# Kernel optimization log

Hardware: AMD Instinct MI355X
Metric: run time of the kernel (lower is better)

## Reference

```python
import jax, jax.numpy as jnp
import numpy as np
import math

EPS = 1e-5  # BatchNorm eps; eval mode with running_mean=0, running_var=1


def maxpool(x, k, p):
    return jax.lax.reduce_window(x, -jnp.inf, jax.lax.max,
                                 (1, 1, k, k), (1, 1, 1, 1),
                                 ((0, 0), (0, 0), (p, p), (p, p)))


def conv1x1(x, w, b=None):
    # x: [B,Cin,H,W], w: [Cout,Cin]
    y = jnp.einsum('oi,bihw->bohw', w, x)
    if b is not None:
        y = y + b[None, :, None, None]
    return y


def bn_eval(x, g, b):
    scale = g / jnp.sqrt(1.0 + EPS)
    return x * scale[None, :, None, None] + b[None, :, None, None]


def setup_inputs() -> dict:
    B, C, H, W = 2, 64, 80, 80
    c1, c2, c3 = 21, 21, 22
    ch = 32  # C//2
    ks = jax.random.split(jax.random.key(0), 16)
    s = 0.05
    inp = {
        'x': jax.random.normal(ks[0], (B, C, H, W), jnp.float32),
        'q1_w': jax.random.normal(ks[1], (c1, c1), jnp.float32) * s,
        'q1_g': jnp.ones((c1,), jnp.float32),
        'q1_b': jnp.zeros((c1,), jnp.float32),
        'q2_w': jax.random.normal(ks[2], (c2, c2), jnp.float32) * s,
        'q2_g': jnp.ones((c2,), jnp.float32),
        'q2_b': jnp.zeros((c2,), jnp.float32),
        'q3_w': jax.random.normal(ks[3], (c3, c3), jnp.float32) * s,
        'q3_g': jnp.ones((c3,), jnp.float32),
        'q3_b': jnp.zeros((c3,), jnp.float32),
        'k_hf_w': jax.random.normal(ks[4], (ch, C), jnp.float32) * s,
        'k_hf_b': jnp.zeros((ch,), jnp.float32),
        'k_lf_w': jax.random.normal(ks[5], (C - ch, C), jnp.float32) * s,
        'k_lf_b': jnp.zeros((C - ch,), jnp.float32),
        'k_fuse_w': jax.random.normal(ks[6], (C, C), jnp.float32) * s,
        'k_fuse_b': jnp.zeros((C,), jnp.float32),
        'v_bn_g': jnp.ones((C,), jnp.float32),
        'v_bn_b': jnp.zeros((C,), jnp.float32),
        'v_w': jax.random.normal(ks[7], (C, C), jnp.float32) * s,
        'v_b': jnp.zeros((C,), jnp.float32),
        'out_w': jax.random.normal(ks[8], (C, C), jnp.float32) * s,
        'out_b': jnp.zeros((C,), jnp.float32),
    }
    return inp


def reference(x, q1_w, q1_g, q1_b, q2_w, q2_g, q2_b, q3_w, q3_g, q3_b,
              k_hf_w, k_hf_b, k_lf_w, k_lf_b, k_fuse_w, k_fuse_b,
              v_bn_g, v_bn_b, v_w, v_b, out_w, out_b):
    B, C, H, W = x.shape
    N = H * W
    c1 = q1_w.shape[0]
    c2 = q2_w.shape[0]
    # Q: ThreeGroupConvQ (split -> 1x1 conv (no bias) -> BN -> ReLU -> concat)
    x1, x2, x3 = jnp.split(x, [c1, c1 + c2], axis=1)
    y1 = jax.nn.relu(bn_eval(conv1x1(x1, q1_w), q1_g, q1_b))
    y2 = jax.nn.relu(bn_eval(conv1x1(x2, q2_w), q2_g, q2_b))
    y3 = jax.nn.relu(bn_eval(conv1x1(x3, q3_w), q3_g, q3_b))
    Q = jnp.concatenate([y1, y2, y3], axis=1)
    # K: ThermalStructureExtractor
    p3 = maxpool(x, 3, 1)
    p5 = maxpool(x, 5, 2)
    low = (p3 + p5) * 0.5
    high = conv1x1(x - low, k_hf_w, k_hf_b)
    lowp = conv1x1(low, k_lf_w, k_lf_b)
    K = conv1x1(jnp.concatenate([high, lowp], axis=1), k_fuse_w, k_fuse_b)
    # V: BN -> 1x1 conv
    V = conv1x1(bn_eval(x, v_bn_g, v_bn_b), v_w, v_b)
    # attention over N = H*W spatial tokens, channel features
    Qc = Q.reshape(B, C, N)
    Kc = K.reshape(B, C, N)
    Vc = V.reshape(B, C, N)
    attn = jax.nn.softmax(
        jnp.einsum('bcn,bcm->bnm', Qc, Kc) / math.sqrt(C), axis=-1)  # [B,N,N]
    out = jnp.einsum('bnm,bcm->bcn', attn, Vc).reshape(B, C, H, W)
    return conv1x1(out, out_w, out_b) + x
```

## Files before the change

kernel.cpp:

```cpp
#include <hip/hip_runtime.h>
#include <hip/hip_bf16.h>


#define BATCH 2
#define CH 64
#define HH 80
#define WW 80
#define NN 6400
#define NT 100
#define KS 10
#define KTPS (NT/KS)
#define EPSV 1e-5f
#define NEGBIG (-1e30f)
#define QP 72
#define LOG2E8 0.18033688f
#define VSP 65

typedef __hip_bfloat16 bf16;
typedef __attribute__((ext_vector_type(8))) short short8;
typedef __attribute__((ext_vector_type(4))) float f4;
#define MFMA16 __builtin_amdgcn_mfma_f32_16x16x32_bf16

__device__ __forceinline__ float b2f(bf16 v){ return __bfloat162float(v); }
__device__ __forceinline__ bf16 f2b(float v){ return __float2bfloat16(v); }
__device__ __forceinline__ ushort f2bu(float v){ return ((__hip_bfloat16_raw)__float2bfloat16(v)).x; }
__device__ __forceinline__ float bu2f(ushort u){
  union { unsigned int i; float f; } w; w.i = ((unsigned int)u) << 16; return w.f;
}
__device__ __forceinline__ unsigned pkbf(float a, float b){
  union { __hip_bfloat162 h2; unsigned u; } cv;
  cv.h2 = __float22bfloat162_rn(make_float2(a, b));
  return cv.u;
}
__device__ __forceinline__ float fexp2(float x){
#if __has_builtin(__builtin_amdgcn_exp2f)
  return __builtin_amdgcn_exp2f(x);
#else
  return exp2f(x);
#endif
}

#define OFF_BIAS 0
#define OFF_WH_B 768
#define OFF_LOW_B (768 + 32768)
#define OFF_Q_B   (OFF_LOW_B + BATCH*CH*NN*2)
#define OFF_K_B   (OFF_Q_B   + BATCH*CH*NN*2)
#define OFF_V_B   (OFF_K_B   + BATCH*CH*NN*2)
#define OFF_P_B   (OFF_V_B   + BATCH*CH*NN*2)
#define OFF_ML_B  (OFF_P_B   + BATCH*NT*KS*4096*2)

__global__ __launch_bounds__(256) void setup_fold(
    const float* __restrict__ q1w, const float* __restrict__ q1g, const float* __restrict__ q1b,
    const float* __restrict__ q2w, const float* __restrict__ q2g, const float* __restrict__ q2b,
    const float* __restrict__ q3w, const float* __restrict__ q3g, const float* __restrict__ q3b,
    const float* __restrict__ khw, const float* __restrict__ khb,
    const float* __restrict__ klw, const float* __restrict__ klb,
    const float* __restrict__ kfw, const float* __restrict__ kfb,
    const float* __restrict__ vg,  const float* __restrict__ vbnb,
    const float* __restrict__ vw,  const float* __restrict__ vb,
    const float* __restrict__ outw,
    float* __restrict__ biasf, bf16* __restrict__ wh)
{
  __shared__ __align__(16) float skf[4096];
  __shared__ __align__(16) float skh[2048];
  __shared__ __align__(16) float skl[2048];
  __shared__ __align__(16) float sow[4096];
  __shared__ __align__(16) float svw[4096];
  __shared__ float sbv[64];

  int tid = threadIdx.x;
  int blk = blockIdx.x;
  #pragma unroll
  for (int i = 0; i < 4; ++i) {
    *(float4*)&skf[(i*256 + tid)*4] = *(const float4*)&kfw[(i*256 + tid)*4];
    *(float4*)&sow[(i*256 + tid)*4] = *(const float4*)&outw[(i*256 + tid)*4];
    *(float4*)&svw[(i*256 + tid)*4] = *(const float4*)&vw[(i*256 + tid)*4];
  }
  #pragma unroll
  for (int i = 0; i < 2; ++i) {
    *(float4*)&skh[(i*256 + tid)*4] = *(const float4*)&khw[(i*256 + tid)*4];
    *(float4*)&skl[(i*256 + tid)*4] = *(const float4*)&klw[(i*256 + tid)*4];
  }
  __syncthreads();

  float rs = rsqrtf(1.0f + EPSV);
  if (tid < 64) {
    int j = tid;
    float bvo = vb[j];
    for (int ci2 = 0; ci2 < 64; ++ci2) bvo += svw[j*64 + ci2] * vbnb[ci2];
    sbv[j] = bvo;
  }

  bf16* wq   = wh;
  bf16* wvp  = wh + 4096;
  bf16* wa1  = wh + 8192;
  bf16* wa2m = wh + 12288;

  int t = blk*256 + tid;
  int ci = t & 63, co = t >> 6;
  int o = ci*64 + co;

  float w = 0.f, g;
  if (co < 21)      { g = q1g[co];    w = (ci < 21)              ? q1w[co*21 + ci]            : 0.f; }
  else if (co < 42) { g = q2g[co-21]; w = (ci >= 21 && ci < 42)  ? q2w[(co-21)*21 + (ci-21)]  : 0.f; }
  else              { g = q3g[co-42]; w = (ci >= 42)             ? q3w[(co-42)*22 + (ci-42)]  : 0.f; }
  wq[o] = f2b(w * g * rs * LOG2E8);

  float a1 = 0.f, a2 = 0.f;
  #pragma unroll
  for (int j = 0; j < 32; ++j) {
    a1 += skf[co*64 + j]      * skh[j*64 + ci];
    a2 += skf[co*64 + 32 + j] * skl[j*64 + ci];
  }
  wa1[o]  = f2b(a1);
  wa2m[o] = f2b(a2 - a1);

  float av = 0.f;
  #pragma unroll
  for (int j = 0; j < 64; ++j)
    av += sow[co*64 + j] * svw[j*64 + ci];
  wvp[o] = f2b(av * vg[ci] * rs);

  if (blk == 0 && tid < 64) {
    int c2 = tid;
    float bq;
    if (c2 < 21)      bq = q1b[c2];
    else if (c2 < 42) bq = q2b[c2-21];
    else              bq = q3b[c2-42];
    biasf[c2] = bq * LOG2E8;
    float bk = kfb[c2];
    #pragma unroll
    for (int j = 0; j < 32; ++j) {
      bk += skf[c2*64 + j]      * khb[j];
      bk += skf[c2*64 + 32 + j] * klb[j];
    }
    biasf[64 + c2] = bk;
    __syncthreads();
  }
  __syncthreads();
  if (blk == 0 && tid < 64) {
    int c2 = tid;
    float bvp = 0.f;
    #pragma unroll
    for (int j = 0; j < 64; ++j) bvp += sow[c2*64 + j] * sbv[j];
    biasf[128 + c2] = bvp;
  }
}

__global__ __launch_bounds__(256) void pool_low(const float* __restrict__ x,
                                                bf16* __restrict__ lowg)
{
  int t4 = (blockIdx.x*256 + threadIdx.x)*4;
  int bc = t4 / NN; int n = t4 % NN;
  int h = n / WW, w0 = n % WW;
  const float* p = x + bc*NN;
  float m5[4], m3[4];
  #pragma unroll
  for (int j=0;j<4;++j){ m5[j]=NEGBIG; m3[j]=NEGBIG; }
  #pragma unroll
  for (int dh = -2; dh <= 2; ++dh) {
    int hh = h + dh; if (hh < 0 || hh >= HH) continue;
    float r[12];
    const float* row = p + hh*WW;
    if (w0 >= 4)      { float4 a = *(const float4*)&row[w0-4]; r[0]=a.x;r[1]=a.y;r[2]=a.z;r[3]=a.w; }
    else              { r[0]=NEGBIG;r[1]=NEGBIG;r[2]=NEGBIG;r[3]=NEGBIG; }
    { float4 a = *(const float4*)&row[w0]; r[4]=a.x;r[5]=a.y;r[6]=a.z;r[7]=a.w; }
    if (w0 + 7 < WW)  { float4 a = *(const float4*)&row[w0+4]; r[8]=a.x;r[9]=a.y;r[10]=a.z;r[11]=a.w; }
    else              { r[8]=NEGBIG;r[9]=NEGBIG;r[10]=NEGBIG;r[11]=NEGBIG; }
    bool in3 = (dh >= -1 && dh <= 1);
    #pragma unroll
    for (int j=0;j<4;++j) {
      float v3 = fmaxf(fmaxf(r[3+j], r[4+j]), r[5+j]);
      float v5 = fmaxf(fmaxf(r[2+j], v3), r[6+j]);
      m5[j] = fmaxf(m5[j], v5);
      if (in3) m3[j] = fmaxf(m3[j], v3);
    }
  }
  ushort4 o;
  o.x = f2bu(0.5f*(m3[0]+m5[0]));
  o.y = f2bu(0.5f*(m3[1]+m5[1]));
  o.z = f2bu(0.5f*(m3[2]+m5[2]));
  o.w = f2bu(0.5f*(m3[3]+m5[3]));
  *(ushort4*)&lowg[t4] = o;
}

__global__ __launch_bounds__(256) void qkv_kernel(
    const float* __restrict__ x, const float* __restrict__ biasf,
    const bf16* __restrict__ wh, const bf16* __restrict__ lowg,
    bf16* __restrict__ qgT, bf16* __restrict__ kgT, bf16* __restrict__ vgc)
{
  __shared__ __align__(16) float xs[64*32];
  __shared__ __align__(16) float lows[64*32];
  __shared__ __align__(16) bf16  wbuf[16384];
  __shared__ ushort vs[64*VSP];
  __shared__ float bias[192];

  int tid = threadIdx.x;
  int blk = blockIdx.x;
  int b = blk / (NT*2);
  int rem = blk % (NT*2);
  int tile = rem >> 1, half = rem & 1;
  int n0 = tile*64 + half*32;

  #pragma unroll
  for (int i = 0; i < 8; ++i) {
    int e = i*256 + tid; int c = e >> 5, p = e & 31;
    xs[c*32 + p]   = x[(b*CH + c)*NN + n0 + p];
    lows[c*32 + p] = b2f(lowg[(b*CH + c)*NN + n0 + p]);
  }
  #pragma unroll
  for (int i = 0; i < 16; ++i)
    ((uint2*)wbuf)[i*256 + tid] = ((const uint2*)wh)[i*256 + tid];
  if (tid < 192) bias[tid] = biasf[tid];
  __syncthreads();

  int co = tid & 63, pg = tid >> 6;
  const bf16* wq   = wbuf;
  const bf16* wvp  = wbuf + 4096;
  const bf16* wa1  = wbuf + 8192;
  const bf16* wa2m = wbuf + 12288;

  {
    float bq = bias[co];
    float4 a0 = make_float4(bq,bq,bq,bq), a1v = a0;
    for (int ci = 0; ci < 64; ++ci) {
      float wv = b2f(wq[ci*64 + co]);
      float4 x0 = *(const float4*)&xs[ci*32 + pg*8];
      float4 x1 = *(const float4*)&xs[ci*32 + pg*8 + 4];
      a0.x += wv*x0.x; a0.y += wv*x0.y; a0.z += wv*x0.z; a0.w += wv*x0.w;
      a1v.x += wv*x1.x; a1v.y += wv*x1.y; a1v.z += wv*x1.z; a1v.w += wv*x1.w;
    }
    float q8[8] = {a0.x,a0.y,a0.z,a0.w,a1v.x,a1v.y,a1v.z,a1v.w};
    #pragma unroll
    for (int j=0;j<8;++j)
      qgT[(size_t)(b*NN + n0 + pg*8 + j)*64 + co] = f2b(fmaxf(q8[j], 0.f));
  }
  {
    float bv = bias[128 + co];
    float4 a0 = make_float4(bv,bv,bv,bv), a1v = a0;
    for (int ci = 0; ci < 64; ++ci) {
      float wv = b2f(wvp[ci*64 + co]);
      float4 x0 = *(const float4*)&xs[ci*32 + pg*8];
      float4 x1 = *(const float4*)&xs[ci*32 + pg*8 + 4];
      a0.x += wv*x0.x; a0.y += wv*x0.y; a0.z += wv*x0.z; a0.w += wv*x0.w;
      a1v.x += wv*x1.x; a1v.y += wv*x1.y; a1v.z += wv*x1.z; a1v.w += wv*x1.w;
    }
    float v8[8] = {a0.x,a0.y,a0.z,a0.w,a1v.x,a1v.y,a1v.z,a1v.w};
    #pragma unroll
    for (int j=0;j<8;++j)
      vs[co*VSP + pg*8 + j] = f2bu(v8[j]);
  }
  __syncthreads();
  {
    int c = tid >> 2, cb = (tid & 3)*8;
    ushort u[8];
    #pragma unroll
    for (int j=0;j<8;++j) u[j] = vs[c*VSP + cb + j];
    uint4 pk;
    pk.x = (uint)u[0] | ((uint)u[1] << 16);
    pk.y = (uint)u[2] | ((uint)u[3] << 16);
    pk.z = (uint)u[4] | ((uint)u[5] << 16);
    pk.w = (uint)u[6] | ((uint)u[7] << 16);
    *(uint4*)&vgc[(size_t)(b*CH + c)*NN + n0 + cb] = pk;
  }
  {
    float bk = bias[64 + co];
    float4 a0 = make_float4(bk,bk,bk,bk), a1v = a0;
    for (int ci = 0; ci < 64; ++ci) {
      float w1 = b2f(wa1[ci*64 + co]);
      float w2 = b2f(wa2m[ci*64 + co]);
      float4 x0 = *(const float4*)&xs[ci*32 + pg*8];
      float4 x1 = *(const float4*)&xs[ci*32 + pg*8 + 4];
      float4 l0 = *(const float4*)&lows[ci*32 + pg*8];
      float4 l1 = *(const float4*)&lows[ci*32 + pg*8 + 4];
      a0.x += w1*x0.x + w2*l0.x; a0.y += w1*x0.y + w2*l0.y;
      a0.z += w1*x0.z + w2*l0.z; a0.w += w1*x0.w + w2*l0.w;
      a1v.x += w1*x1.x + w2*l1.x; a1v.y += w1*x1.y + w2*l1.y;
      a1v.z += w1*x1.z + w2*l1.z; a1v.w += w1*x1.w + w2*l1.w;
    }
    float k8[8] = {a0.x,a0.y,a0.z,a0.w,a1v.x,a1v.y,a1v.z,a1v.w};
    #pragma unroll
    for (int j=0;j<8;++j)
      kgT[(size_t)(b*NN + n0 + pg*8 + j)*64 + co] = f2b(k8[j]);
  }
}

__global__ __launch_bounds__(256) void attn_partial(
    const bf16* __restrict__ qgT, const bf16* __restrict__ kgT, const bf16* __restrict__ vgc,
    ushort* __restrict__ part, float* __restrict__ pml)
{
  __shared__ __align__(16) char smem[27648];
  __shared__ float lred[256];
  bf16* Qld = (bf16*)smem;
  bf16* Pld = (bf16*)smem;
  bf16* Kld = (bf16*)(smem + 9216);
  bf16* Vld = (bf16*)(smem + 18432);

  int tid = threadIdx.x;
  int blk = blockIdx.x;
  int b = blk / (NT*KS);
  int rem = blk % (NT*KS);
  int tile = rem / KS, split = rem % KS;
  int n0 = tile*64;
  int wv = tid >> 6, lane = tid & 63, ln = lane & 15, quad = lane >> 4;
  int arow = (wv*16 + ln)*QP;

  #pragma unroll
  for (int i = 0; i < 4; ++i) {
    int f = (i*256 + tid)*4; int n = f >> 6, c = f & 63;
    *(uint2*)&Qld[n*QP + c] = *(const uint2*)&qgT[(size_t)(b*NN + n0 + n)*64 + c];
  }
  __syncthreads();
  short8 bq[4][2];
  #pragma unroll
  for (int nt = 0; nt < 4; ++nt) {
    bq[nt][0] = *(const short8*)&Qld[(nt*16 + ln)*QP + quad*8];
    bq[nt][1] = *(const short8*)&Qld[(nt*16 + ln)*QP + 32 + quad*8];
  }

  f4 accO[4];
  float lacc[4];
  #pragma unroll
  for (int t=0;t<4;++t) accO[t] = (f4){0.f,0.f,0.f,0.f};
  #pragma unroll
  for (int nt=0;nt<4;++nt) lacc[nt] = 0.f;

  uint2 kreg[4], vreg[4];
  int mbase = split*KTPS*64;
  #pragma unroll
  for (int i = 0; i < 4; ++i) {
    int f = (i*256 + tid)*4; int rr = f >> 6, cc = f & 63;
    kreg[i] = *(const uint2*)&kgT[(size_t)(b*NN + mbase + rr)*64 + cc];
    vreg[i] = *(const uint2*)&vgc[(size_t)(b*CH + rr)*NN + mbase + cc];
  }

  for (int kt = 0; kt < KTPS; ++kt) {
    __syncthreads();
    #pragma unroll
    for (int i = 0; i < 4; ++i) {
      int f = (i*256 + tid)*4; int rr = f >> 6, cc = f & 63;
      *(uint2*)&Kld[rr*QP + cc] = kreg[i];
      *(uint2*)&Vld[rr*QP + cc] = vreg[i];
    }
    __syncthreads();
    if (kt + 1 < KTPS) {
      int m0 = mbase + (kt+1)*64;
      #pragma unroll
      for (int i = 0; i < 4; ++i) {
        int f = (i*256 + tid)*4; int rr = f >> 6, cc = f & 63;
        kreg[i] = *(const uint2*)&kgT[(size_t)(b*NN + m0 + rr)*64 + cc];
        vreg[i] = *(const uint2*)&vgc[(size_t)(b*CH + rr)*NN + m0 + cc];
      }
    }

    short8 ak0 = *(const short8*)&Kld[arow + quad*8];
    short8 ak1 = *(const short8*)&Kld[arow + 32 + quad*8];
    f4 accS[4];
    #pragma unroll
    for (int nt = 0; nt < 4; ++nt) {
      f4 z = (f4){0.f,0.f,0.f,0.f};
      z = MFMA16(ak0, bq[nt][0], z, 0, 0, 0);
      accS[nt] = MFMA16(ak1, bq[nt][1], z, 0, 0, 0);
    }
    #pragma unroll
    for (int nt = 0; nt < 4; ++nt) {
      float p0 = fexp2(accS[nt][0]), p1 = fexp2(accS[nt][1]);
      float p2 = fexp2(accS[nt][2]), p3 = fexp2(accS[nt][3]);
      lacc[nt] += (p0 + p1) + (p2 + p3);
      uint2 pk;
      pk.x = pkbf(p0, p1);
      pk.y = pkbf(p2, p3);
      *(uint2*)&Pld[(nt*16 + ln)*QP + wv*16 + quad*4] = pk;
    }
    __syncthreads();

    short8 ap0 = *(const short8*)&Pld[arow + quad*8];
    short8 ap1 = *(const short8*)&Pld[arow + 32 + quad*8];
    #pragma unroll
    for (int t = 0; t < 4; ++t) {
      short8 bv0 = *(const short8*)&Vld[(t*16+ln)*QP + quad*8];
      short8 bv1 = *(const short8*)&Vld[(t*16+ln)*QP + 32 + quad*8];
      accO[t] = MFMA16(ap0, bv0, accO[t], 0, 0, 0);
      accO[t] = MFMA16(ap1, bv1, accO[t], 0, 0, 0);
    }
  }

  size_t pbase = ((size_t)(b*NT + tile)*KS + split)*4096;
  ushort* pp = part + pbase;
  #pragma unroll
  for (int t = 0; t < 4; ++t) {
    uint2 pk;
    pk.x = pkbf(accO[t][0], accO[t][1]);
    pk.y = pkbf(accO[t][2], accO[t][3]);
    *(uint2*)&pp[(t*16 + ln)*64 + wv*16 + quad*4] = pk;
  }
  #pragma unroll
  for (int nt = 0; nt < 4; ++nt) {
    float s = lacc[nt];
    s += __shfl_xor(s, 16);
    s += __shfl_xor(s, 32);
    if (quad == 0) lred[wv*64 + nt*16 + ln] = s;
  }
  __syncthreads();
  if (tid < 64) {
    size_t mlb = ((size_t)(b*NT + tile)*KS + split)*64;
    pml[mlb + tid] = (lred[tid] + lred[64 + tid]) + (lred[128 + tid] + lred[192 + tid]);
  }
}

__global__ __launch_bounds__(256) void attn_reduce(
    const ushort* __restrict__ part, const float* __restrict__ pml,
    const float* __restrict__ x, const float* __restrict__ outb,
    float* __restrict__ out)
{
  __shared__ float linv[64];
  __shared__ float ob[64];

  int tid = threadIdx.x;
  int blk = blockIdx.x;
  int b = blk / NT, tile = blk % NT;
  size_t base = (size_t)(b*NT + tile)*KS;

  if (tid < 64) {
    float l = 0.f;
    #pragma unroll
    for (int s=0;s<KS;++s) l += pml[(base+s)*64 + tid];
    linv[tid] = 1.0f / l;
    ob[tid] = outb[tid];
  }
  __syncthreads();

  #pragma unroll
  for (int j = 0; j < 4; ++j) {
    int idx = j*256 + tid;
    int c = idx >> 4, q = idx & 15;
    float a0=0.f, a1=0.f, a2=0.f, a3=0.f;
    #pragma unroll
    for (int s = 0; s < KS; ++s) {
      uint2 v = *(const uint2*)&part[(base+s)*4096 + (size_t)c*64 + q*4];
      a0 += bu2f((ushort)(v.x & 0xffff)); a1 += bu2f((ushort)(v.x >> 16));
      a2 += bu2f((ushort)(v.y & 0xffff)); a3 += bu2f((ushort)(v.y >> 16));
    }
    int nl = q*4;
    size_t gidx = (size_t)(b*CH + c)*NN + tile*64 + nl;
    float4 xv = *(const float4*)&x[gidx];
    float bc = ob[c];
    float4 o;
    o.x = a0*linv[nl+0] + bc + xv.x;
    o.y = a1*linv[nl+1] + bc + xv.y;
    o.z = a2*linv[nl+2] + bc + xv.z;
    o.w = a3*linv[nl+3] + bc + xv.w;
    *(float4*)&out[gidx] = o;
  }
}

extern "C" void kernel_launch(void* const* d_in, const int* in_sizes, int n_in,
                              void* d_out, int out_size, void* d_ws, size_t ws_size,
                              hipStream_t stream) {
  const float* x    = (const float*)d_in[0];
  const float* q1w  = (const float*)d_in[1];
  const float* q1g  = (const float*)d_in[2];
  const float* q1b  = (const float*)d_in[3];
  const float* q2w  = (const float*)d_in[4];
  const float* q2g  = (const float*)d_in[5];
  const float* q2b  = (const float*)d_in[6];
  const float* q3w  = (const float*)d_in[7];
  const float* q3g  = (const float*)d_in[8];
  const float* q3b  = (const float*)d_in[9];
  const float* khw  = (const float*)d_in[10];
  const float* khb  = (const float*)d_in[11];
  const float* klw  = (const float*)d_in[12];
  const float* klb  = (const float*)d_in[13];
  const float* kfw  = (const float*)d_in[14];
  const float* kfb  = (const float*)d_in[15];
  const float* vbg  = (const float*)d_in[16];
  const float* vbb  = (const float*)d_in[17];
  const float* vw   = (const float*)d_in[18];
  const float* vb   = (const float*)d_in[19];
  const float* outw = (const float*)d_in[20];
  const float* outb = (const float*)d_in[21];

  char*   wsb  = (char*)d_ws;
  float*  biasf= (float*)(wsb + OFF_BIAS);
  bf16*   wh   = (bf16*)(wsb + OFF_WH_B);
  bf16*   lowg = (bf16*)(wsb + OFF_LOW_B);
  bf16*   qgT  = (bf16*)(wsb + OFF_Q_B);
  bf16*   kgT  = (bf16*)(wsb + OFF_K_B);
  bf16*   vgc  = (bf16*)(wsb + OFF_V_B);
  ushort* part = (ushort*)(wsb + OFF_P_B);
  float*  pml  = (float*)(wsb + OFF_ML_B);

  hipLaunchKernelGGL(setup_fold, dim3(16), dim3(256), 0, stream,
                     q1w,q1g,q1b,q2w,q2g,q2b,q3w,q3g,q3b,
                     khw,khb,klw,klb,kfw,kfb,vbg,vbb,vw,vb,outw, biasf, wh);
  hipLaunchKernelGGL(pool_low, dim3(BATCH*CH*NN/1024), dim3(256), 0, stream, x, lowg);
  hipLaunchKernelGGL(qkv_kernel, dim3(BATCH*NT*2), dim3(256), 0, stream,
                     x, biasf, wh, lowg, qgT, kgT, vgc);
  hipLaunchKernelGGL(attn_partial, dim3(BATCH*NT*KS), dim3(256), 0, stream,
                     qgT, kgT, vgc, part, pml);
  hipLaunchKernelGGL(attn_reduce, dim3(BATCH*NT), dim3(256), 0, stream,
                     part, pml, x, outb, (float*)d_out);
}
```

Before: 171.2 us.

## Fuse attention split-K partials and reduction into one 1024-thread block kernel

```diff
diff --git a/kernel.cpp b/kernel.cpp
--- a/kernel.cpp
+++ b/kernel.cpp
@@ -8,13 +8,15 @@
 #define WW 80
 #define NN 6400
 #define NT 100
-#define KS 10
-#define KTPS (NT/KS)
+#define NG 4
+#define KTPS 25
 #define EPSV 1e-5f
 #define NEGBIG (-1e30f)
 #define QP 72
 #define LOG2E8 0.18033688f
 #define VSP 65
+#define GREG 27648
+#define OPF 65
 
 typedef __hip_bfloat16 bf16;
 typedef __attribute__((ext_vector_type(8))) short short8;
@@ -24,9 +26,6 @@
 __device__ __forceinline__ float b2f(bf16 v){ return __bfloat162float(v); }
 __device__ __forceinline__ bf16 f2b(float v){ return __float2bfloat16(v); }
 __device__ __forceinline__ ushort f2bu(float v){ return ((__hip_bfloat16_raw)__float2bfloat16(v)).x; }
-__device__ __forceinline__ float bu2f(ushort u){
-  union { unsigned int i; float f; } w; w.i = ((unsigned int)u) << 16; return w.f;
-}
 __device__ __forceinline__ unsigned pkbf(float a, float b){
   union { __hip_bfloat162 h2; unsigned u; } cv;
   cv.h2 = __float22bfloat162_rn(make_float2(a, b));
@@ -46,10 +45,9 @@
 #define OFF_Q_B   (OFF_LOW_B + BATCH*CH*NN*2)
 #define OFF_K_B   (OFF_Q_B   + BATCH*CH*NN*2)
 #define OFF_V_B   (OFF_K_B   + BATCH*CH*NN*2)
-#define OFF_P_B   (OFF_V_B   + BATCH*CH*NN*2)
-#define OFF_ML_B  (OFF_P_B   + BATCH*NT*KS*4096*2)
-
-__global__ __launch_bounds__(256) void setup_fold(
+
+__global__ __launch_bounds__(256) void setup_pool(
+    const float* __restrict__ x,
     const float* __restrict__ q1w, const float* __restrict__ q1g, const float* __restrict__ q1b,
     const float* __restrict__ q2w, const float* __restrict__ q2g, const float* __restrict__ q2b,
     const float* __restrict__ q3w, const float* __restrict__ q3g, const float* __restrict__ q3b,
@@ -59,129 +57,104 @@
     const float* __restrict__ vg,  const float* __restrict__ vbnb,
     const float* __restrict__ vw,  const float* __restrict__ vb,
     const float* __restrict__ outw,
-    float* __restrict__ biasf, bf16* __restrict__ wh)
+    float* __restrict__ biasf, bf16* __restrict__ wh, bf16* __restrict__ lowg)
 {
-  __shared__ __align__(16) float skf[4096];
-  __shared__ __align__(16) float skh[2048];
-  __shared__ __align__(16) float skl[2048];
-  __shared__ __align__(16) float sow[4096];
-  __shared__ __align__(16) float svw[4096];
   __shared__ float sbv[64];
-
   int tid = threadIdx.x;
   int blk = blockIdx.x;
-  #pragma unroll
-  for (int i = 0; i < 4; ++i) {
-    *(float4*)&skf[(i*256 + tid)*4] = *(const float4*)&kfw[(i*256 + tid)*4];
-    *(float4*)&sow[(i*256 + tid)*4] = *(const float4*)&outw[(i*256 + tid)*4];
-    *(float4*)&svw[(i*256 + tid)*4] = *(const float4*)&vw[(i*256 + tid)*4];
-  }
-  #pragma unroll
-  for (int i = 0; i < 2; ++i) {
-    *(float4*)&skh[(i*256 + tid)*4] = *(const float4*)&khw[(i*256 + tid)*4];
-    *(float4*)&skl[(i*256 + tid)*4] = *(const float4*)&klw[(i*256 + tid)*4];
-  }
-  __syncthreads();
-
-  float rs = rsqrtf(1.0f + EPSV);
-  if (tid < 64) {
-    int j = tid;
-    float bvo = vb[j];
-    for (int ci2 = 0; ci2 < 64; ++ci2) bvo += svw[j*64 + ci2] * vbnb[ci2];
-    sbv[j] = bvo;
-  }
-
-  bf16* wq   = wh;
-  bf16* wvp  = wh + 4096;
-  bf16* wa1  = wh + 8192;
-  bf16* wa2m = wh + 12288;
-
-  int t = blk*256 + tid;
-  int ci = t & 63, co = t >> 6;
-  int o = ci*64 + co;
-
-  float w = 0.f, g;
-  if (co < 21)      { g = q1g[co];    w = (ci < 21)              ? q1w[co*21 + ci]            : 0.f; }
-  else if (co < 42) { g = q2g[co-21]; w = (ci >= 21 && ci < 42)  ? q2w[(co-21)*21 + (ci-21)]  : 0.f; }
-  else              { g = q3g[co-42]; w = (ci >= 42)             ? q3w[(co-42)*22 + (ci-42)]  : 0.f; }
-  wq[o] = f2b(w * g * rs * LOG2E8);
-
-  float a1 = 0.f, a2 = 0.f;
-  #pragma unroll
-  for (int j = 0; j < 32; ++j) {
-    a1 += skf[co*64 + j]      * skh[j*64 + ci];
-    a2 += skf[co*64 + 32 + j] * skl[j*64 + ci];
-  }
-  wa1[o]  = f2b(a1);
-  wa2m[o] = f2b(a2 - a1);
-
-  float av = 0.f;
-  #pragma unroll
-  for (int j = 0; j < 64; ++j)
-    av += sow[co*64 + j] * svw[j*64 + ci];
-  wvp[o] = f2b(av * vg[ci] * rs);
-
-  if (blk == 0 && tid < 64) {
-    int c2 = tid;
-    float bq;
-    if (c2 < 21)      bq = q1b[c2];
-    else if (c2 < 42) bq = q2b[c2-21];
-    else              bq = q3b[c2-42];
-    biasf[c2] = bq * LOG2E8;
-    float bk = kfb[c2];
-    #pragma unroll
+
+  if (blk < 16) {
+    float rs = rsqrtf(1.0f + EPSV);
+    bf16* wq   = wh;
+    bf16* wvp  = wh + 4096;
+    bf16* wa1  = wh + 8192;
+    bf16* wa2m = wh + 12288;
+
+    int t = blk*256 + tid;
+    int ci = t & 63, co = t >> 6;
+    int o = ci*64 + co;
+
+    float w = 0.f, g;
+    if (co < 21)      { g = q1g[co];    w = (ci < 21)              ? q1w[co*21 + ci]            : 0.f; }
+    else if (co < 42) { g = q2g[co-21]; w = (ci >= 21 && ci < 42)  ? q2w[(co-21)*21 + (ci-21)]  : 0.f; }
+    else              { g = q3g[co-42]; w = (ci >= 42)             ? q3w[(co-42)*22 + (ci-42)]  : 0.f; }
+    wq[o] = f2b(w * g * rs * LOG2E8);
+
+    float a1 = 0.f, a2 = 0.f, av = 0.f;
+    #pragma unroll 8
     for (int j = 0; j < 32; ++j) {
-      bk += skf[c2*64 + j]      * khb[j];
-      bk += skf[c2*64 + 32 + j] * klb[j];
-    }
-    biasf[64 + c2] = bk;
-    __syncthreads();
-  }
-  __syncthreads();
-  if (blk == 0 && tid < 64) {
-    int c2 = tid;
-    float bvp = 0.f;
-    #pragma unroll
-    for (int j = 0; j < 64; ++j) bvp += sow[c2*64 + j] * sbv[j];
-    biasf[128 + c2] = bvp;
-  }
-}
-
-__global__ __launch_bounds__(256) void pool_low(const float* __restrict__ x,
-                                                bf16* __restrict__ lowg)
-{
-  int t4 = (blockIdx.x*256 + threadIdx.x)*4;
-  int bc = t4 / NN; int n = t4 % NN;
-  int h = n / WW, w0 = n % WW;
-  const float* p = x + bc*NN;
-  float m5[4], m3[4];
-  #pragma unroll
-  for (int j=0;j<4;++j){ m5[j]=NEGBIG; m3[j]=NEGBIG; }
-  #pragma unroll
-  for (int dh = -2; dh <= 2; ++dh) {
-    int hh = h + dh; if (hh < 0 || hh >= HH) continue;
-    float r[12];
-    const float* row = p + hh*WW;
-    if (w0 >= 4)      { float4 a = *(const float4*)&row[w0-4]; r[0]=a.x;r[1]=a.y;r[2]=a.z;r[3]=a.w; }
-    else              { r[0]=NEGBIG;r[1]=NEGBIG;r[2]=NEGBIG;r[3]=NEGBIG; }
-    { float4 a = *(const float4*)&row[w0]; r[4]=a.x;r[5]=a.y;r[6]=a.z;r[7]=a.w; }
-    if (w0 + 7 < WW)  { float4 a = *(const float4*)&row[w0+4]; r[8]=a.x;r[9]=a.y;r[10]=a.z;r[11]=a.w; }
-    else              { r[8]=NEGBIG;r[9]=NEGBIG;r[10]=NEGBIG;r[11]=NEGBIG; }
-    bool in3 = (dh >= -1 && dh <= 1);
-    #pragma unroll
-    for (int j=0;j<4;++j) {
-      float v3 = fmaxf(fmaxf(r[3+j], r[4+j]), r[5+j]);
-      float v5 = fmaxf(fmaxf(r[2+j], v3), r[6+j]);
-      m5[j] = fmaxf(m5[j], v5);
-      if (in3) m3[j] = fmaxf(m3[j], v3);
-    }
-  }
-  ushort4 o;
-  o.x = f2bu(0.5f*(m3[0]+m5[0]));
-  o.y = f2bu(0.5f*(m3[1]+m5[1]));
-  o.z = f2bu(0.5f*(m3[2]+m5[2]));
-  o.w = f2bu(0.5f*(m3[3]+m5[3]));
-  *(ushort4*)&lowg[t4] = o;
+      a1 += kfw[co*64 + j]      * khw[j*64 + ci];
+      a2 += kfw[co*64 + 32 + j] * klw[j*64 + ci];
+    }
+    #pragma unroll 8
+    for (int j = 0; j < 64; ++j)
+      av += outw[co*64 + j] * vw[j*64 + ci];
+    wa1[o]  = f2b(a1);
+    wa2m[o] = f2b(a2 - a1);
+    wvp[o]  = f2b(av * vg[ci] * rs);
+
+    if (blk == 0) {
+      if (tid < 64) {
+        int j = tid;
+        float bvo = vb[j];
+        for (int c2 = 0; c2 < 64; ++c2) bvo += vw[j*64 + c2] * vbnb[c2];
+        sbv[j] = bvo;
+      }
+      __syncthreads();
+      if (tid < 64) {
+        int c2 = tid;
+        float bq;
+        if (c2 < 21)      bq = q1b[c2];
+        else if (c2 < 42) bq = q2b[c2-21];
+        else              bq = q3b[c2-42];
+        biasf[c2] = bq * LOG2E8;
+        float bk = kfb[c2];
+        #pragma unroll 8
+        for (int j = 0; j < 32; ++j) {
+          bk += kfw[c2*64 + j]      * khb[j];
+          bk += kfw[c2*64 + 32 + j] * klb[j];
+        }
+        biasf[64 + c2] = bk;
+        float bvp = 0.f;
+        #pragma unroll 8
+        for (int j = 0; j < 64; ++j) bvp += outw[c2*64 + j] * sbv[j];
+        biasf[128 + c2] = bvp;
+      }
+    }
+  } else {
+    int t4 = ((blk - 16)*256 + tid)*4;
+    int bc = t4 / NN; int n = t4 % NN;
+    int h = n / WW, w0 = n % WW;
+    const float* p = x + bc*NN;
+    float m5[4], m3[4];
+    #pragma unroll
+    for (int j=0;j<4;++j){ m5[j]=NEGBIG; m3[j]=NEGBIG; }
+    #pragma unroll
+    for (int dh = -2; dh <= 2; ++dh) {
+      int hh = h + dh; if (hh < 0 || hh >= HH) continue;
+      float r[12];
+      const float* row = p + hh*WW;
+      if (w0 >= 4)      { float4 a = *(const float4*)&row[w0-4]; r[0]=a.x;r[1]=a.y;r[2]=a.z;r[3]=a.w; }
+      else              { r[0]=NEGBIG;r[1]=NEGBIG;r[2]=NEGBIG;r[3]=NEGBIG; }
+      { float4 a = *(const float4*)&row[w0]; r[4]=a.x;r[5]=a.y;r[6]=a.z;r[7]=a.w; }
+      if (w0 + 7 < WW)  { float4 a = *(const float4*)&row[w0+4]; r[8]=a.x;r[9]=a.y;r[10]=a.z;r[11]=a.w; }
+      else              { r[8]=NEGBIG;r[9]=NEGBIG;r[10]=NEGBIG;r[11]=NEGBIG; }
+      bool in3 = (dh >= -1 && dh <= 1);
+      #pragma unroll
+      for (int j=0;j<4;++j) {
+        float v3 = fmaxf(fmaxf(r[3+j], r[4+j]), r[5+j]);
+        float v5 = fmaxf(fmaxf(r[2+j], v3), r[6+j]);
+        m5[j] = fmaxf(m5[j], v5);
+        if (in3) m3[j] = fmaxf(m3[j], v3);
+      }
+    }
+    ushort4 o;
+    o.x = f2bu(0.5f*(m3[0]+m5[0]));
+    o.y = f2bu(0.5f*(m3[1]+m5[1]));
+    o.z = f2bu(0.5f*(m3[2]+m5[2]));
+    o.w = f2bu(0.5f*(m3[3]+m5[3]));
+    *(ushort4*)&lowg[t4] = o;
+  }
 }
 
 __global__ __launch_bounds__(256) void qkv_kernel(
@@ -285,29 +258,30 @@
   }
 }
 
-__global__ __launch_bounds__(256) void attn_partial(
+__global__ __launch_bounds__(1024, 4) void attn_mono(
     const bf16* __restrict__ qgT, const bf16* __restrict__ kgT, const bf16* __restrict__ vgc,
-    ushort* __restrict__ part, float* __restrict__ pml)
+    const float* __restrict__ x, const float* __restrict__ outb,
+    float* __restrict__ out)
 {
-  __shared__ __align__(16) char smem[27648];
-  __shared__ float lred[256];
-  bf16* Qld = (bf16*)smem;
-  bf16* Pld = (bf16*)smem;
-  bf16* Kld = (bf16*)(smem + 9216);
-  bf16* Vld = (bf16*)(smem + 18432);
+  __shared__ __align__(16) char sm[120064];
+  bf16* Qld = (bf16*)sm;
+  float* linv = (float*)(sm + 9216 + NG*GREG);
 
   int tid = threadIdx.x;
-  int blk = blockIdx.x;
-  int b = blk / (NT*KS);
-  int rem = blk % (NT*KS);
-  int tile = rem / KS, split = rem % KS;
+  int g  = tid >> 8;
+  int gt = tid & 255;
+  int b = blockIdx.x / NT, tile = blockIdx.x % NT;
   int n0 = tile*64;
-  int wv = tid >> 6, lane = tid & 63, ln = lane & 15, quad = lane >> 4;
+  int wv = gt >> 6, lane = gt & 63, ln = lane & 15, quad = lane >> 4;
   int arow = (wv*16 + ln)*QP;
 
-  #pragma unroll
-  for (int i = 0; i < 4; ++i) {
-    int f = (i*256 + tid)*4; int n = f >> 6, c = f & 63;
+  char* gbase = sm + 9216 + g*GREG;
+  bf16* Kld = (bf16*)gbase;
+  bf16* Vld = (bf16*)(gbase + 9216);
+  bf16* Pld = (bf16*)(gbase + 18432);
+
+  {
+    int f = tid*4; int n = f >> 6, c = f & 63;
     *(uint2*)&Qld[n*QP + c] = *(const uint2*)&qgT[(size_t)(b*NN + n0 + n)*64 + c];
   }
   __syncthreads();
@@ -326,10 +300,10 @@
   for (int nt=0;nt<4;++nt) lacc[nt] = 0.f;
 
   uint2 kreg[4], vreg[4];
-  int mbase = split*KTPS*64;
+  int mbase = g*KTPS*64;
   #pragma unroll
   for (int i = 0; i < 4; ++i) {
-    int f = (i*256 + tid)*4; int rr = f >> 6, cc = f & 63;
+    int f = (i*256 + gt)*4; int rr = f >> 6, cc = f & 63;
     kreg[i] = *(const uint2*)&kgT[(size_t)(b*NN + mbase + rr)*64 + cc];
     vreg[i] = *(const uint2*)&vgc[(size_t)(b*CH + rr)*NN + mbase + cc];
   }
@@ -338,7 +312,7 @@
     __syncthreads();
     #pragma unroll
     for (int i = 0; i < 4; ++i) {
-      int f = (i*256 + tid)*4; int rr = f >> 6, cc = f & 63;
+      int f = (i*256 + gt)*4; int rr = f >> 6, cc = f & 63;
       *(uint2*)&Kld[rr*QP + cc] = kreg[i];
       *(uint2*)&Vld[rr*QP + cc] = vreg[i];
     }
@@ -347,7 +321,7 @@
       int m0 = mbase + (kt+1)*64;
       #pragma unroll
       for (int i = 0; i < 4; ++i) {
-        int f = (i*256 + tid)*4; int rr = f >> 6, cc = f & 63;
+        int f = (i*256 + gt)*4; int rr = f >> 6, cc = f & 63;
         kreg[i] = *(const uint2*)&kgT[(size_t)(b*NN + m0 + rr)*64 + cc];
         vreg[i] = *(const uint2*)&vgc[(size_t)(b*CH + rr)*NN + m0 + cc];
       }
@@ -385,66 +359,48 @@
     }
   }
 
-  size_t pbase = ((size_t)(b*NT + tile)*KS + split)*4096;
-  ushort* pp = part + pbase;
+  __syncthreads();
+  float* Og    = (float*)gbase;
+  float* lgred = (float*)(gbase + 16896);
   #pragma unroll
   for (int t = 0; t < 4; ++t) {
-    uint2 pk;
-    pk.x = pkbf(accO[t][0], accO[t][1]);
-    pk.y = pkbf(accO[t][2], accO[t][3]);
-    *(uint2*)&pp[(t*16 + ln)*64 + wv*16 + quad*4] = pk;
+    #pragma unroll
+    for (int r = 0; r < 4; ++r)
+      Og[(wv*16 + quad*4 + r)*OPF + t*16 + ln] = accO[t][r];
   }
   #pragma unroll
   for (int nt = 0; nt < 4; ++nt) {
     float s = lacc[nt];
     s += __shfl_xor(s, 16);
     s += __shfl_xor(s, 32);
-    if (quad == 0) lred[wv*64 + nt*16 + ln] = s;
-  }
-  __syncthreads();
-  if (tid < 64) {
-    size_t mlb = ((size_t)(b*NT + tile)*KS + split)*64;
-    pml[mlb + tid] = (lred[tid] + lred[64 + tid]) + (lred[128 + tid] + lred[192 + tid]);
-  }
-}
-
-__global__ __launch_bounds__(256) void attn_reduce(
-    const ushort* __restrict__ part, const float* __restrict__ pml,
-    const float* __restrict__ x, const float* __restrict__ outb,
-    float* __restrict__ out)
-{
-  __shared__ float linv[64];
-  __shared__ float ob[64];
-
-  int tid = threadIdx.x;
-  int blk = blockIdx.x;
-  int b = blk / NT, tile = blk % NT;
-  size_t base = (size_t)(b*NT + tile)*KS;
-
+    if (quad == 0) lgred[wv*64 + nt*16 + ln] = s;
+  }
+  __syncthreads();
   if (tid < 64) {
     float l = 0.f;
     #pragma unroll
-    for (int s=0;s<KS;++s) l += pml[(base+s)*64 + tid];
+    for (int g2 = 0; g2 < NG; ++g2) {
+      const float* lr = (const float*)(sm + 9216 + g2*GREG + 16896);
+      l += (lr[tid] + lr[64 + tid]) + (lr[128 + tid] + lr[192 + tid]);
+    }
     linv[tid] = 1.0f / l;
-    ob[tid] = outb[tid];
-  }
-  __syncthreads();
-
-  #pragma unroll
-  for (int j = 0; j < 4; ++j) {
-    int idx = j*256 + tid;
-    int c = idx >> 4, q = idx & 15;
+  }
+  __syncthreads();
+  {
+    int c = tid >> 4, q = tid & 15;
+    int nl = q*4;
     float a0=0.f, a1=0.f, a2=0.f, a3=0.f;
     #pragma unroll
-    for (int s = 0; s < KS; ++s) {
-      uint2 v = *(const uint2*)&part[(base+s)*4096 + (size_t)c*64 + q*4];
-      a0 += bu2f((ushort)(v.x & 0xffff)); a1 += bu2f((ushort)(v.x >> 16));
-      a2 += bu2f((ushort)(v.y & 0xffff)); a3 += bu2f((ushort)(v.y >> 16));
-    }
-    int nl = q*4;
-    size_t gidx = (size_t)(b*CH + c)*NN + tile*64 + nl;
+    for (int g2 = 0; g2 < NG; ++g2) {
+      const float* og = (const float*)(sm + 9216 + g2*GREG);
+      a0 += og[(nl+0)*OPF + c];
+      a1 += og[(nl+1)*OPF + c];
+      a2 += og[(nl+2)*OPF + c];
+      a3 += og[(nl+3)*OPF + c];
+    }
+    size_t gidx = (size_t)(b*CH + c)*NN + n0 + nl;
     float4 xv = *(const float4*)&x[gidx];
-    float bc = ob[c];
+    float bc = outb[c];
     float4 o;
     o.x = a0*linv[nl+0] + bc + xv.x;
     o.y = a1*linv[nl+1] + bc + xv.y;
@@ -487,17 +443,13 @@
   bf16*   qgT  = (bf16*)(wsb + OFF_Q_B);
   bf16*   kgT  = (bf16*)(wsb + OFF_K_B);
   bf16*   vgc  = (bf16*)(wsb + OFF_V_B);
-  ushort* part = (ushort*)(wsb + OFF_P_B);
-  float*  pml  = (float*)(wsb + OFF_ML_B);
-
-  hipLaunchKernelGGL(setup_fold, dim3(16), dim3(256), 0, stream,
-                     q1w,q1g,q1b,q2w,q2g,q2b,q3w,q3g,q3b,
-                     khw,khb,klw,klb,kfw,kfb,vbg,vbb,vw,vb,outw, biasf, wh);
-  hipLaunchKernelGGL(pool_low, dim3(BATCH*CH*NN/1024), dim3(256), 0, stream, x, lowg);
+
+  hipLaunchKernelGGL(setup_pool, dim3(16 + BATCH*CH*NN/1024), dim3(256), 0, stream,
+                     x, q1w,q1g,q1b,q2w,q2g,q2b,q3w,q3g,q3b,
+                     khw,khb,klw,klb,kfw,kfb,vbg,vbb,vw,vb,outw,
+                     biasf, wh, lowg);
   hipLaunchKernelGGL(qkv_kernel, dim3(BATCH*NT*2), dim3(256), 0, stream,
                      x, biasf, wh, lowg, qgT, kgT, vgc);
-  hipLaunchKernelGGL(attn_partial, dim3(BATCH*NT*KS), dim3(256), 0, stream,
-                     qgT, kgT, vgc, part, pml);
-  hipLaunchKernelGGL(attn_reduce, dim3(BATCH*NT), dim3(256), 0, stream,
-                     part, pml, x, outb, (float*)d_out);
-}
+  hipLaunchKernelGGL(attn_mono, dim3(BATCH*NT), dim3(1024), 0, stream,
+                     qgT, kgT, vgc, x, outb, (float*)d_out);
+}
```

New measurement: 178.7 us. 1.04x slower.
